# Performance work log

Hardware: AMD Instinct MI355X
Metric: run time of the kernel (lower is better)

## Reference

```python
import jax, jax.numpy as jnp
import numpy as np

B, H, S, D = 2, 16, 2048, 64  # depth = dmodel / num_heads
DMODEL = H * D


def setup_inputs() -> dict:
    key = jax.random.key(0)
    kq, kk, kv, kw = jax.random.split(key, 4)
    Q = jax.random.normal(kq, (B, H, S, D), dtype=jnp.float32)
    K = jax.random.normal(kk, (B, H, S, D), dtype=jnp.float32)
    V = jax.random.normal(kv, (B, H, S, D), dtype=jnp.float32)
    W = jax.random.normal(kw, (DMODEL, DMODEL), dtype=jnp.float32) * (1.0 / np.sqrt(DMODEL))
    b = jnp.zeros((DMODEL,), dtype=jnp.float32)
    return {"Q": Q, "K": K, "V": V, "W": W, "b": b}


def reference(Q, K, V, W, b):
    depth = Q.shape[-1]
    # scores: (B, H, S, S) -- full score matrix, matching the original math
    scores = jnp.einsum('bhqd,bhkd->bhqk', Q, K) / jnp.sqrt(jnp.float32(depth))
    attn = jax.nn.softmax(scores, axis=-1)
    vals = jnp.einsum('bhqk,bhkd->bhqd', attn, V)          # (B, H, S, D)
    vals = jnp.transpose(vals, (0, 2, 1, 3))               # (B, S, H, D)
    concat = vals.reshape(vals.shape[0], vals.shape[1], -1)  # (B, S, dmodel)
    return concat @ W + b
```

## Files before the change

### kernel.cpp

```cpp
#include <hip/hip_runtime.h>
#include <hip/hip_bf16.h>


typedef float  f32x16 __attribute__((ext_vector_type(16)));
typedef float  f32x4v __attribute__((ext_vector_type(4)));
typedef float  f32x2v __attribute__((ext_vector_type(2)));
typedef __bf16 bf16x8 __attribute__((ext_vector_type(8)));
typedef __bf16 bf16x4 __attribute__((ext_vector_type(4)));
typedef __bf16 bf16x2 __attribute__((ext_vector_type(2)));

static constexpr int Bn = 2, Hn = 16, Sn = 2048, Dn = 64, DM = 1024;
static constexpr size_t QKV_ELEMS = (size_t)Bn * Hn * Sn * Dn;

#define QSCALE 0.18033688011112042f

#define LGKM_BARRIER() do {                                  \
    asm volatile("s_waitcnt lgkmcnt(0)" ::: "memory");       \
    __builtin_amdgcn_s_barrier();                            \
  } while (0)

#if __has_builtin(__builtin_amdgcn_cvt_pk_bf16_f32)
static __device__ __forceinline__ unsigned pack2(float a, float b) {
  bf16x2 t = __builtin_amdgcn_cvt_pk_bf16_f32(a, b);
  union { bf16x2 v; unsigned u; } c; c.v = t; return c.u;
}
#else
static __device__ __forceinline__ unsigned pack2(float a, float b) {
  union { __bf16 h; unsigned short s; } ua, ub;
  ua.h = (__bf16)a; ub.h = (__bf16)b;
  return (unsigned)ua.s | ((unsigned)ub.s << 16);
}
#endif

static __device__ __forceinline__ void unzip8(const unsigned* wds, bf16x8* r0, bf16x8* r1) {
  union { unsigned u[4]; bf16x8 v; } a, b;
#pragma unroll
  for (int i = 0; i < 4; ++i) {
    unsigned lo = wds[2 * i], hi = wds[2 * i + 1];
    a.u[i] = (lo & 0xffffu) | (hi << 16);
    b.u[i] = (lo >> 16) | (hi & 0xffff0000u);
  }
  *r0 = a.v; *r1 = b.v;
}

__global__ __launch_bounds__(256) void convert_all(
    const float* __restrict__ k,
    const float* __restrict__ v, const float* __restrict__ w,
    __bf16* __restrict__ ko,
    __bf16* __restrict__ vt, __bf16* __restrict__ wt) {
  __shared__ __bf16 T[64][74];
  const int bid = blockIdx.x, t = threadIdx.x;

  if (bid < 2048) {
    size_t i = ((size_t)bid * 256 + t) * 8;
    f32x4v a = *(const f32x4v*)(k + i);
    f32x4v b = *(const f32x4v*)(k + i + 4);
    bf16x8 o;
#pragma unroll
    for (int j = 0; j < 4; ++j) { o[j] = (__bf16)a[j]; o[4 + j] = (__bf16)b[j]; }
    *(bf16x8*)(ko + i) = o;
    return;
  }

  const float* s0;
  __bf16* dst0 = nullptr;
  size_t dst_stride = 0;
  int nt_ = 0, kt_ = 0;
  const bool isW = (bid >= 3072);
  {
    const int r = t >> 2, c0 = (t & 3) * 16;
    if (!isW) {
      const int idx = bid - 2048;
      const int kv0 = (idx & 31) * 64, bh = idx >> 5;
      s0 = v + ((size_t)bh * Sn + kv0 + r) * Dn + c0;
      dst0 = vt + (size_t)bh * Dn * Sn + kv0;
      dst_stride = Sn;
    } else {
      const int idx = bid - 3072;
      nt_ = (idx & 15) * 64; kt_ = (idx >> 4) * 64;
      s0 = w + (size_t)(kt_ + r) * DM + nt_ + c0;
    }
    union { bf16x8 v8; unsigned u[4]; } o0, o1;
#pragma unroll
    for (int i = 0; i < 2; ++i) {
      f32x4v f = *(const f32x4v*)(s0 + i * 4);
#pragma unroll
      for (int j = 0; j < 4; ++j) o0.v8[i * 4 + j] = (__bf16)f[j];
    }
#pragma unroll
    for (int i = 0; i < 2; ++i) {
      f32x4v f = *(const f32x4v*)(s0 + 8 + i * 4);
#pragma unroll
      for (int j = 0; j < 4; ++j) o1.v8[i * 4 + j] = (__bf16)f[j];
    }
#pragma unroll
    for (int j = 0; j < 4; ++j) {
      *(unsigned*)&T[r][c0 + 2 * j]     = o0.u[j];
      *(unsigned*)&T[r][c0 + 8 + 2 * j] = o1.u[j];
    }
  }
  __syncthreads();
  const int rp = t >> 3, k0 = (t & 7) * 8;
  unsigned wds[8];
#pragma unroll
  for (int i = 0; i < 8; ++i) wds[i] = *(const unsigned*)&T[k0 + i][2 * rp];
  bf16x8 r0, r1; unzip8(wds, &r0, &r1);
  if (!isW) {
    __bf16* d0 = dst0 + (size_t)(2 * rp) * dst_stride + k0;
    *(bf16x8*)d0 = r0;
    *(bf16x8*)(d0 + dst_stride) = r1;
  } else {
    const int n0 = nt_ + 2 * rp;
    __bf16* d0 = wt + ((size_t)(n0 >> 5) * 128 + (kt_ >> 3) + (t & 7)) * 256
                    + (n0 & 31) * 8;
    *(bf16x8*)d0 = r0;
    *(bf16x8*)(d0 + 8) = r1;
  }
}

__global__ __launch_bounds__(512, 4) void attn(
    const float* __restrict__ Qf, const __bf16* __restrict__ Kb,
    const __bf16* __restrict__ Vtg, __bf16* __restrict__ Cc) {
  const int tid = threadIdx.x;
  const int wave = tid >> 6, lane = tid & 63;
  const int ln = lane & 31, g = lane >> 5;
  const int qg = wave >> 1, kh = wave & 1;
  const int f = blockIdx.x;
  const int swz = (f & 7) * 64 + (f >> 3);
  const int qb = swz & 15, h = (swz >> 4) & 15, bz = swz >> 8;

  __shared__ __bf16 Ks[2][128][72];
  __shared__ __bf16 Vs[2][64][136];

  const size_t hoff = (size_t)(bz * Hn + h) * Sn * Dn;
  const float*  Qp = Qf + hoff + (size_t)(qb * 128 + qg * 32) * Dn;
  const __bf16* Kp = Kb + hoff;
  const __bf16* Vp = Vtg + hoff;

  bf16x8 qf[4];
#pragma unroll
  for (int ks = 0; ks < 4; ++ks) {
    const float* qp = Qp + (size_t)ln * Dn + ks * 16 + g * 8;
    f32x4v f0 = *(const f32x4v*)qp;
    f32x4v f1 = *(const f32x4v*)(qp + 4);
#pragma unroll
    for (int j = 0; j < 4; ++j) {
      qf[ks][j]     = (__bf16)(f0[j] * QSCALE);
      qf[ks][4 + j] = (__bf16)(f1[j] * QSCALE);
    }
  }

  const int kr = tid >> 2, kc = (tid & 3) * 16;
  const int vr = tid >> 3, vc = (tid & 7) * 16;
  const __bf16* kbase = Kp + (size_t)kr * Dn + kc;
  const __bf16* vbase = Vp + (size_t)vr * Sn + vc;

  bf16x8 k0r = *(const bf16x8*)kbase, k1r = *(const bf16x8*)(kbase + 8);
  bf16x8 v0r = *(const bf16x8*)vbase, v1r = *(const bf16x8*)(vbase + 8);
  {
    *(bf16x8*)&Ks[0][kr][kc]     = k0r;
    *(bf16x8*)&Ks[0][kr][kc + 8] = k1r;
    union { bf16x8 v; bf16x4 h[2]; } u0, u1; u0.v = v0r; u1.v = v1r;
    union { bf16x4 h[2]; bf16x8 v; } w0, w1;
    w0.h[0] = u0.h[0]; w0.h[1] = u1.h[0];
    w1.h[0] = u0.h[1]; w1.h[1] = u1.h[1];
    *(bf16x8*)&Vs[0][vr][vc]     = w0.v;
    *(bf16x8*)&Vs[0][vr][vc + 8] = w1.v;
  }
  k0r = *(const bf16x8*)(kbase + (size_t)128 * Dn);
  k1r = *(const bf16x8*)(kbase + (size_t)128 * Dn + 8);
  v0r = *(const bf16x8*)(vbase + 128);
  v1r = *(const bf16x8*)(vbase + 128 + 8);
  LGKM_BARRIER();

  f32x16 O0 = {}, O1 = {};
  float Lown = 0.0f;
  constexpr int NT = Sn / 128;

  for (int kt = 0; kt < NT; ++kt) {
    const int buf = kt & 1;

    unsigned w[16];
#pragma unroll
    for (int m = 0; m < 2; ++m) {
      bf16x8 kf[4];
#pragma unroll
      for (int ks = 0; ks < 4; ++ks)
        kf[ks] = *(const bf16x8*)&Ks[buf][kh * 64 + m * 32 + ln][ks * 16 + g * 8];

      f32x16 s = {};
      __builtin_amdgcn_s_setprio(1);
#pragma unroll
      for (int ks = 0; ks < 4; ++ks)
        s = __builtin_amdgcn_mfma_f32_32x32x16_bf16(kf[ks], qf[ks], s, 0, 0, 0);
      __builtin_amdgcn_s_setprio(0);

      float p[16];
#pragma unroll
      for (int r = 0; r < 16; ++r) p[r] = __builtin_amdgcn_exp2f(s[r]);
      f32x2v s2 = {0.0f, 0.0f};
#pragma unroll
      for (int tt = 0; tt < 8; ++tt) { f32x2v t2 = {p[2 * tt], p[2 * tt + 1]}; s2 += t2; }
      Lown += s2[0] + s2[1];
#pragma unroll
      for (int tt = 0; tt < 8; ++tt) w[m * 8 + tt] = pack2(p[2 * tt], p[2 * tt + 1]);
    }

    if (kt + 1 < NT) {
      const int nb = buf ^ 1;
      *(bf16x8*)&Ks[nb][kr][kc]     = k0r;
      *(bf16x8*)&Ks[nb][kr][kc + 8] = k1r;
      union { bf16x8 v; bf16x4 h[2]; } u0, u1; u0.v = v0r; u1.v = v1r;
      union { bf16x4 h[2]; bf16x8 v; } w0, w1;
      w0.h[0] = u0.h[0]; w0.h[1] = u1.h[0];
      w1.h[0] = u0.h[1]; w1.h[1] = u1.h[1];
      *(bf16x8*)&Vs[nb][vr][vc]     = w0.v;
      *(bf16x8*)&Vs[nb][vr][vc + 8] = w1.v;
      if (kt + 2 < NT) {
        const __bf16* kp = kbase + (size_t)(kt + 2) * 128 * Dn;
        k0r = *(const bf16x8*)kp; k1r = *(const bf16x8*)(kp + 8);
        const __bf16* vp = vbase + (kt + 2) * 128;
        v0r = *(const bf16x8*)vp; v1r = *(const bf16x8*)(vp + 8);
      }
    }

    __builtin_amdgcn_s_setprio(1);
#pragma unroll
    for (int s4 = 0; s4 < 4; ++s4) {
      const int cb = kh * 64 + s4 * 16 + g * 8;
      bf16x8 vf0 = *(const bf16x8*)&Vs[buf][ln][cb];
      bf16x8 vf1 = *(const bf16x8*)&Vs[buf][32 + ln][cb];
      union { unsigned u[4]; bf16x8 v; } pu;
      pu.u[0] = w[s4 * 4 + 0];
      pu.u[1] = w[s4 * 4 + 1];
      pu.u[2] = w[s4 * 4 + 2];
      pu.u[3] = w[s4 * 4 + 3];
      O0 = __builtin_amdgcn_mfma_f32_32x32x16_bf16(vf0, pu.v, O0, 0, 0, 0);
      O1 = __builtin_amdgcn_mfma_f32_32x32x16_bf16(vf1, pu.v, O1, 0, 0, 0);
    }
    __builtin_amdgcn_s_setprio(0);

    LGKM_BARRIER();
  }

  const float Lred = Lown + __shfl_xor(Lown, 32);
  float* Ex = (float*)Ks;
  const int slot = (qg * 64 + lane) * 36;
  if (kh == 1) {
#pragma unroll
    for (int i = 0; i < 4; ++i) {
      f32x4v t = {O0[4 * i], O0[4 * i + 1], O0[4 * i + 2], O0[4 * i + 3]};
      *(f32x4v*)&Ex[slot + 4 * i] = t;
    }
#pragma unroll
    for (int i = 0; i < 4; ++i) {
      f32x4v t = {O1[4 * i], O1[4 * i + 1], O1[4 * i + 2], O1[4 * i + 3]};
      *(f32x4v*)&Ex[slot + 16 + 4 * i] = t;
    }
    Ex[slot + 32] = Lred;
  }
  __syncthreads();
  __bf16* T = (__bf16*)Vs;
  if (kh == 0) {
    float inv;
#pragma unroll
    for (int i = 0; i < 4; ++i) {
      f32x4v t = *(const f32x4v*)&Ex[slot + 4 * i];
#pragma unroll
      for (int c = 0; c < 4; ++c) O0[4 * i + c] += t[c];
    }
#pragma unroll
    for (int i = 0; i < 4; ++i) {
      f32x4v t = *(const f32x4v*)&Ex[slot + 16 + 4 * i];
#pragma unroll
      for (int c = 0; c < 4; ++c) O1[4 * i + c] += t[c];
    }
    inv = 1.0f / (Lred + Ex[slot + 32]);
#pragma unroll
    for (int dh = 0; dh < 2; ++dh) {
#pragma unroll
      for (int a = 0; a < 4; ++a) {
        const f32x16 O = dh ? O1 : O0;
        bf16x4 t4;
#pragma unroll
        for (int c = 0; c < 4; ++c) t4[c] = (__bf16)(O[4 * a + c] * inv);
        *(bf16x4*)&T[(qg * 32 + ln) * 72 + dh * 32 + 8 * a + 4 * g] = t4;
      }
    }
  }
  __syncthreads();
  const int q0 = qb * 128;
#pragma unroll
  for (int i = 0; i < 2; ++i) {
    const int rq = i * 64 + (tid >> 3);
    const int c8 = (tid & 7) * 8;
    bf16x8 o = *(const bf16x8*)&T[rq * 72 + c8];
    const int m = bz * Sn + q0 + rq;
    const int kg = h * 8 + (tid & 7);
    size_t base = ((size_t)(m >> 5) * 128 + kg) * 256 + (m & 31) * 8;
    *(bf16x8*)&Cc[base] = o;
  }
}

__global__ __launch_bounds__(512, 4) void proj(
    const __bf16* __restrict__ A2, const __bf16* __restrict__ Wt2,
    const float* __restrict__ bias, float* __restrict__ out) {
  const int tid = threadIdx.x, wave = tid >> 6, lane = tid & 63;
  const int ln = lane & 31, g = lane >> 5;
  const int mq = wave >> 1, nh = wave & 1;
  const int f = blockIdx.x;
  const int idx = f >> 3;
  const int bn = idx & 15;
  const int bm = (f & 7) * 4 + (idx >> 4);

  const int mg = bm * 4 + mq;
  const int ng = bn * 2 + nh;
  const __bf16* Ab = A2  + (size_t)mg * 128 * 256 + (size_t)ln * 8;
  const __bf16* Wb = Wt2 + (size_t)ng * 128 * 256 + (size_t)ln * 8;

  f32x16 acc = {};
#pragma unroll 4
  for (int kt = 0; kt < 16; ++kt) {
#pragma unroll
    for (int ks = 0; ks < 4; ++ks) {
      const size_t off = (size_t)(kt * 8 + ks * 2 + g) * 256;
      bf16x8 af = *(const bf16x8*)(Ab + off);
      bf16x8 wf = *(const bf16x8*)(Wb + off);
      acc = __builtin_amdgcn_mfma_f32_32x32x16_bf16(af, wf, acc, 0, 0, 0);
    }
  }
  const float bv = bias[bn * 64 + nh * 32 + ln];
#pragma unroll
  for (int r = 0; r < 16; ++r) {
    int row = bm * 128 + mq * 32 + (r & 3) + 8 * (r >> 2) + 4 * g;
    out[(size_t)row * DM + bn * 64 + nh * 32 + ln] = acc[r] + bv;
  }
}

extern "C" void kernel_launch(void* const* d_in, const int* in_sizes, int n_in,
                              void* d_out, int out_size, void* d_ws, size_t ws_size,
                              hipStream_t stream) {
  const float* Q = (const float*)d_in[0];
  const float* K = (const float*)d_in[1];
  const float* V = (const float*)d_in[2];
  const float* W = (const float*)d_in[3];
  const float* b = (const float*)d_in[4];
  float* out = (float*)d_out;

  __bf16* ws  = (__bf16*)d_ws;
  __bf16* Kb  = ws;
  __bf16* Vtg = Kb + QKV_ELEMS;
  __bf16* Cc  = Vtg + QKV_ELEMS;
  __bf16* Wt  = Cc + QKV_ELEMS;

  convert_all<<<dim3(3328, 1, 1), 256, 0, stream>>>(K, V, W, Kb, Vtg, Wt);
  attn<<<dim3(512, 1, 1), 512, 0, stream>>>(Q, Kb, Vtg, Cc);
  proj<<<dim3(512, 1, 1), 512, 0, stream>>>(Cc, Wt, b, out);
}
```

Measured before the change: 159.4 us.

## Fuse K bf16 conversion into attention loads and split attention per batch

Drops the separate K float-to-bf16 pass from the conversion kernel. The attention kernel now loads K as fp32 and converts it in registers before storing to LDS, which saves one round-trip of K through global memory. Attention is also launched twice, once per batch, with 256 blocks each instead of one 512-block launch. The trade-offs are doubled K global load bytes in the inner loop, more prefetch registers, and an extra kernel launch with fewer blocks per launch.

```diff
diff --git a/kernel.cpp b/kernel.cpp
--- a/kernel.cpp
+++ b/kernel.cpp
@@ -43,40 +43,25 @@
   *r0 = a.v; *r1 = b.v;
 }
 
-__global__ __launch_bounds__(256) void convert_all(
-    const float* __restrict__ k,
+__global__ __launch_bounds__(256) void convert_vw(
     const float* __restrict__ v, const float* __restrict__ w,
-    __bf16* __restrict__ ko,
     __bf16* __restrict__ vt, __bf16* __restrict__ wt) {
   __shared__ __bf16 T[64][74];
   const int bid = blockIdx.x, t = threadIdx.x;
 
-  if (bid < 2048) {
-    size_t i = ((size_t)bid * 256 + t) * 8;
-    f32x4v a = *(const f32x4v*)(k + i);
-    f32x4v b = *(const f32x4v*)(k + i + 4);
-    bf16x8 o;
-#pragma unroll
-    for (int j = 0; j < 4; ++j) { o[j] = (__bf16)a[j]; o[4 + j] = (__bf16)b[j]; }
-    *(bf16x8*)(ko + i) = o;
-    return;
-  }
-
   const float* s0;
   __bf16* dst0 = nullptr;
-  size_t dst_stride = 0;
   int nt_ = 0, kt_ = 0;
-  const bool isW = (bid >= 3072);
+  const bool isW = (bid >= 1024);
   {
     const int r = t >> 2, c0 = (t & 3) * 16;
     if (!isW) {
-      const int idx = bid - 2048;
+      const int idx = bid;
       const int kv0 = (idx & 31) * 64, bh = idx >> 5;
       s0 = v + ((size_t)bh * Sn + kv0 + r) * Dn + c0;
       dst0 = vt + (size_t)bh * Dn * Sn + kv0;
-      dst_stride = Sn;
     } else {
-      const int idx = bid - 3072;
+      const int idx = bid - 1024;
       nt_ = (idx & 15) * 64; kt_ = (idx >> 4) * 64;
       s0 = w + (size_t)(kt_ + r) * DM + nt_ + c0;
     }
@@ -106,9 +91,9 @@
   for (int i = 0; i < 8; ++i) wds[i] = *(const unsigned*)&T[k0 + i][2 * rp];
   bf16x8 r0, r1; unzip8(wds, &r0, &r1);
   if (!isW) {
-    __bf16* d0 = dst0 + (size_t)(2 * rp) * dst_stride + k0;
+    __bf16* d0 = dst0 + (size_t)(2 * rp) * Sn + k0;
     *(bf16x8*)d0 = r0;
-    *(bf16x8*)(d0 + dst_stride) = r1;
+    *(bf16x8*)(d0 + Sn) = r1;
   } else {
     const int n0 = nt_ + 2 * rp;
     __bf16* d0 = wt + ((size_t)(n0 >> 5) * 128 + (kt_ >> 3) + (t & 7)) * 256
@@ -119,22 +104,22 @@
 }
 
 __global__ __launch_bounds__(512, 4) void attn(
-    const float* __restrict__ Qf, const __bf16* __restrict__ Kb,
-    const __bf16* __restrict__ Vtg, __bf16* __restrict__ Cc) {
+    const float* __restrict__ Qf, const float* __restrict__ Kf,
+    const __bf16* __restrict__ Vtg, __bf16* __restrict__ Cc, int bz) {
   const int tid = threadIdx.x;
   const int wave = tid >> 6, lane = tid & 63;
   const int ln = lane & 31, g = lane >> 5;
   const int qg = wave >> 1, kh = wave & 1;
   const int f = blockIdx.x;
-  const int swz = (f & 7) * 64 + (f >> 3);
-  const int qb = swz & 15, h = (swz >> 4) & 15, bz = swz >> 8;
+  const int swz = (f & 7) * 32 + (f >> 3);
+  const int qb = swz & 15, h = swz >> 4;
 
   __shared__ __bf16 Ks[2][128][72];
   __shared__ __bf16 Vs[2][64][136];
 
   const size_t hoff = (size_t)(bz * Hn + h) * Sn * Dn;
   const float*  Qp = Qf + hoff + (size_t)(qb * 128 + qg * 32) * Dn;
-  const __bf16* Kp = Kb + hoff;
+  const float*  Kp = Kf + hoff;
   const __bf16* Vp = Vtg + hoff;
 
   bf16x8 qf[4];
@@ -152,14 +137,25 @@
 
   const int kr = tid >> 2, kc = (tid & 3) * 16;
   const int vr = tid >> 3, vc = (tid & 7) * 16;
-  const __bf16* kbase = Kp + (size_t)kr * Dn + kc;
-  const __bf16* vbase = Vp + (size_t)vr * Sn + vc;
-
-  bf16x8 k0r = *(const bf16x8*)kbase, k1r = *(const bf16x8*)(kbase + 8);
-  bf16x8 v0r = *(const bf16x8*)vbase, v1r = *(const bf16x8*)(vbase + 8);
+  const float*  kbasef = Kp + (size_t)kr * Dn + kc;
+  const __bf16* vbase  = Vp + (size_t)vr * Sn + vc;
+
+  f32x4v ka0, ka1, ka2, ka3;
+  bf16x8 v0r, v1r;
   {
-    *(bf16x8*)&Ks[0][kr][kc]     = k0r;
-    *(bf16x8*)&Ks[0][kr][kc + 8] = k1r;
+    ka0 = *(const f32x4v*)(kbasef);
+    ka1 = *(const f32x4v*)(kbasef + 4);
+    ka2 = *(const f32x4v*)(kbasef + 8);
+    ka3 = *(const f32x4v*)(kbasef + 12);
+    bf16x8 kx0, kx1;
+#pragma unroll
+    for (int j = 0; j < 4; ++j) {
+      kx0[j] = (__bf16)ka0[j]; kx0[4 + j] = (__bf16)ka1[j];
+      kx1[j] = (__bf16)ka2[j]; kx1[4 + j] = (__bf16)ka3[j];
+    }
+    *(bf16x8*)&Ks[0][kr][kc]     = kx0;
+    *(bf16x8*)&Ks[0][kr][kc + 8] = kx1;
+    v0r = *(const bf16x8*)vbase; v1r = *(const bf16x8*)(vbase + 8);
     union { bf16x8 v; bf16x4 h[2]; } u0, u1; u0.v = v0r; u1.v = v1r;
     union { bf16x4 h[2]; bf16x8 v; } w0, w1;
     w0.h[0] = u0.h[0]; w0.h[1] = u1.h[0];
@@ -167,8 +163,10 @@
     *(bf16x8*)&Vs[0][vr][vc]     = w0.v;
     *(bf16x8*)&Vs[0][vr][vc + 8] = w1.v;
   }
-  k0r = *(const bf16x8*)(kbase + (size_t)128 * Dn);
-  k1r = *(const bf16x8*)(kbase + (size_t)128 * Dn + 8);
+  ka0 = *(const f32x4v*)(kbasef + (size_t)128 * Dn);
+  ka1 = *(const f32x4v*)(kbasef + (size_t)128 * Dn + 4);
+  ka2 = *(const f32x4v*)(kbasef + (size_t)128 * Dn + 8);
+  ka3 = *(const f32x4v*)(kbasef + (size_t)128 * Dn + 12);
   v0r = *(const bf16x8*)(vbase + 128);
   v1r = *(const bf16x8*)(vbase + 128 + 8);
   LGKM_BARRIER();
@@ -208,8 +206,14 @@
 
     if (kt + 1 < NT) {
       const int nb = buf ^ 1;
-      *(bf16x8*)&Ks[nb][kr][kc]     = k0r;
-      *(bf16x8*)&Ks[nb][kr][kc + 8] = k1r;
+      bf16x8 kx0, kx1;
+#pragma unroll
+      for (int j = 0; j < 4; ++j) {
+        kx0[j] = (__bf16)ka0[j]; kx0[4 + j] = (__bf16)ka1[j];
+        kx1[j] = (__bf16)ka2[j]; kx1[4 + j] = (__bf16)ka3[j];
+      }
+      *(bf16x8*)&Ks[nb][kr][kc]     = kx0;
+      *(bf16x8*)&Ks[nb][kr][kc + 8] = kx1;
       union { bf16x8 v; bf16x4 h[2]; } u0, u1; u0.v = v0r; u1.v = v1r;
       union { bf16x4 h[2]; bf16x8 v; } w0, w1;
       w0.h[0] = u0.h[0]; w0.h[1] = u1.h[0];
@@ -217,8 +221,9 @@
       *(bf16x8*)&Vs[nb][vr][vc]     = w0.v;
       *(bf16x8*)&Vs[nb][vr][vc + 8] = w1.v;
       if (kt + 2 < NT) {
-        const __bf16* kp = kbase + (size_t)(kt + 2) * 128 * Dn;
-        k0r = *(const bf16x8*)kp; k1r = *(const bf16x8*)(kp + 8);
+        const float* kp = kbasef + (size_t)(kt + 2) * 128 * Dn;
+        ka0 = *(const f32x4v*)kp;       ka1 = *(const f32x4v*)(kp + 4);
+        ka2 = *(const f32x4v*)(kp + 8); ka3 = *(const f32x4v*)(kp + 12);
         const __bf16* vp = vbase + (kt + 2) * 128;
         v0r = *(const bf16x8*)vp; v1r = *(const bf16x8*)(vp + 8);
       }
@@ -348,12 +353,12 @@
   float* out = (float*)d_out;
 
   __bf16* ws  = (__bf16*)d_ws;
-  __bf16* Kb  = ws;
-  __bf16* Vtg = Kb + QKV_ELEMS;
+  __bf16* Vtg = ws;
   __bf16* Cc  = Vtg + QKV_ELEMS;
   __bf16* Wt  = Cc + QKV_ELEMS;
 
-  convert_all<<<dim3(3328, 1, 1), 256, 0, stream>>>(K, V, W, Kb, Vtg, Wt);
-  attn<<<dim3(512, 1, 1), 512, 0, stream>>>(Q, Kb, Vtg, Cc);
+  convert_vw<<<dim3(1280, 1, 1), 256, 0, stream>>>(V, W, Vtg, Wt);
+  attn<<<dim3(256, 1, 1), 512, 0, stream>>>(Q, K, Vtg, Cc, 0);
+  attn<<<dim3(256, 1, 1), 512, 0, stream>>>(Q, K, Vtg, Cc, 1);
   proj<<<dim3(512, 1, 1), 512, 0, stream>>>(Cc, Wt, b, out);
 }
```

Measured after the change: 165.1 us. 3.6% more time.
